# Kernel tuning notes

Hardware: AMD Instinct MI355X
Metric: run time of the kernel (lower is better)

The kernel has to match this reference:

```python
import jax, jax.numpy as jnp
import numpy as np

N_USER = 100000
N_ITEM = 50000
N = N_USER + N_ITEM
E = 1000000
D = 64
B = 4096
GAMMA = -0.45
ZETA = 1.05
LAMBDA0 = 1e-4
REG_WEIGHT = 1e-4


def setup_inputs() -> dict:
    key = jax.random.key(0)
    ks = jax.random.split(key, 20)
    s = 1.0 / np.sqrt(D)
    inp = {
        'features': jax.random.normal(ks[0], (N, D), jnp.float32) * 0.1,
        'row': jax.random.randint(ks[1], (E,), 0, N, jnp.int32),
        'col': jax.random.randint(ks[2], (E,), 0, N, jnp.int32),
        'users': jax.random.randint(ks[3], (B,), 0, N_USER, jnp.int32),
        'items': jax.random.randint(ks[4], (B,), 0, N_ITEM, jnp.int32),
        'neg_items': jax.random.randint(ks[5], (B,), 0, N_ITEM, jnp.int32),
        'u0': jax.random.uniform(ks[6], (E, 1), jnp.float32, 1e-7, 1.0 - 1e-7),
        'u1': jax.random.uniform(ks[7], (E, 1), jnp.float32, 1e-7, 1.0 - 1e-7),
        'temperature': jnp.full((1,), 0.5, jnp.float32),
        'W_nb0': jax.random.normal(ks[8], (D, D), jnp.float32) * s,
        'b_nb0': jnp.zeros((D,), jnp.float32),
        'W_self0': jax.random.normal(ks[9], (D, D), jnp.float32) * s,
        'b_self0': jnp.zeros((D,), jnp.float32),
        'W_att0': jax.random.normal(ks[10], (2 * D, 1), jnp.float32) * s,
        'b_att0': jnp.zeros((1,), jnp.float32),
        'W_nb1': jax.random.normal(ks[11], (D, D), jnp.float32) * s,
        'b_nb1': jnp.zeros((D,), jnp.float32),
        'W_self1': jax.random.normal(ks[12], (D, D), jnp.float32) * s,
        'b_self1': jnp.zeros((D,), jnp.float32),
        'W_att1': jax.random.normal(ks[13], (2 * D, 1), jnp.float32) * s,
        'b_att1': jnp.zeros((1,), jnp.float32),
    }
    return inp


def _edge_layer(x, row, col, u, Wn, bn, Ws, bs, Wa, ba, temp):
    # edge-gather attention MLP: [E, D] gathers + small GEMMs
    h_nb = jax.nn.relu(x[row] @ Wn + bn)
    h_self = jax.nn.relu(x[col] @ Ws + bs)
    log_alpha = jnp.concatenate([h_nb, h_self], axis=1) @ Wa + ba  # [E, 1]
    # hard-concrete sample (training=True): logistic noise + stretch + clip
    noise = jnp.log(u) - jnp.log1p(-u)
    gate = jax.nn.sigmoid((noise + log_alpha) / temp)
    mask = jnp.clip(gate * (ZETA - GAMMA) + GAMMA, 0.0, 1.0)[:, 0]  # [E]
    # sparse symmetric degree normalization
    rowsum = jax.ops.segment_sum(mask, row, num_segments=N) + 1e-6
    d_inv_sqrt = jnp.clip(rowsum ** -0.5, 0.0, 10.0)
    vals = mask * d_inv_sqrt[row] * d_inv_sqrt[col]
    # SpMM: x_next[r] = sum_e vals[e] * x[col[e]]
    x_next = jax.ops.segment_sum(vals[:, None] * x[col], row, num_segments=N)
    return x_next, log_alpha


def reference(features, row, col, users, items, neg_items, u0, u1, temperature,
              W_nb0, b_nb0, W_self0, b_self0, W_att0, b_att0,
              W_nb1, b_nb1, W_self1, b_self1, W_att1, b_att1):
    t = temperature[0]
    x1, w0 = _edge_layer(features, row, col, u0, W_nb0, b_nb0, W_self0, b_self0, W_att0, b_att0, t)
    x2, w1 = _edge_layer(x1, row, col, u1, W_nb1, b_nb1, W_self1, b_self1, W_att1, b_att1, t)
    xs = features + x1 + x2  # sum(embedsLst)
    x_user, x_item = xs[:N_USER], xs[N_USER:]
    anc, pos, neg = x_user[users], x_item[items], x_item[neg_items]
    pos_scores = jnp.sum(anc * pos, axis=1)
    neg_scores = jnp.sum(anc * neg, axis=1)
    bpr = -jnp.mean(jnp.log(jax.nn.sigmoid(pos_scores - neg_scores) + 1e-5))
    params = [W_nb0, b_nb0, W_self0, b_self0, W_att0, b_att0,
              W_nb1, b_nb1, W_self1, b_self1, W_att1, b_att1]
    reg = sum(jnp.sum(p * p) for p in params) * REG_WEIGHT
    lt = jnp.log(-GAMMA / ZETA)
    l0 = (jnp.mean(jax.nn.sigmoid(w0 - t * lt)) + jnp.mean(jax.nn.sigmoid(w1 - t * lt))) * LAMBDA0
    return bpr + reg + l0
```

## Files before the change

kernel.cpp:

```cpp
#include <hip/hip_runtime.h>
#include <hip/hip_bf16.h>

#define N_TOT   150000
#define N_USER  100000
#define E_TOT   1000000
#define B_TOT   4096
#define D_DIM   64

#define NSCAN_PAD   150016
#define BKT_SHIFT   10
#define BKT_ROWS    (1 << BKT_SHIFT)
#define NBKT        ((N_TOT + BKT_ROWS - 1) / BKT_ROWS)
#define BKT_CAP     8192
#define BIN_CHUNK   4096
#define NBIN_BLOCKS ((E_TOT + BIN_CHUNK - 1) / BIN_CHUNK)
#define COL_MASK    0x3FFFF

typedef short short8v  __attribute__((ext_vector_type(8)));
typedef float float4v  __attribute__((ext_vector_type(4)));

__device__ __forceinline__ float b2f(unsigned int lo16)
{
    union { unsigned int u; float f; } c; c.u = lo16 << 16; return c.f;
}
__device__ __forceinline__ unsigned short f2b(float f)
{
    union { float f; unsigned int u; } c; c.f = f;
    unsigned int u = c.u + 0x7FFFu + ((c.u >> 16) & 1u);
    return (unsigned short)(u >> 16);
}
__device__ __forceinline__ unsigned short f2h(float f)
{
    union { _Float16 h; unsigned short u; } c; c.h = (_Float16)f; return c.u;
}
__device__ __forceinline__ float h2f(unsigned short u)
{
    union { unsigned short u; _Float16 h; } c; c.u = u; return (float)c.h;
}
__device__ __forceinline__ int   f_as_i(float f) { union { float f; int i; } c; c.f = f; return c.i; }
__device__ __forceinline__ float i_as_f(int i)   { union { int i; float f; } c; c.i = i; return c.f; }

__global__ void prep_kernel(const float4* __restrict__ in, ushort4* __restrict__ out, int n4,
                            const float* __restrict__ Wn0, const float* __restrict__ Ws0,
                            const float* __restrict__ Wn1, const float* __restrict__ Ws1,
                            unsigned short* __restrict__ wpk)
{
    if (blockIdx.x < 1024) {
        for (int i = blockIdx.x * 256 + threadIdx.x; i < n4; i += 1024 * 256) {
            float4 v = in[i];
            ushort4 o;
            o.x = f2b(v.x); o.y = f2b(v.y); o.z = f2b(v.z); o.w = f2b(v.w);
            out[i] = o;
        }
        return;
    }
    int f = (blockIdx.x - 1024) * 256 + threadIdx.x;
    if (f >= 2048) return;
    const float* W[4] = {Wn0, Ws0, Wn1, Ws1};
    int m   = f >> 9;
    int rem = f & 511;
    int kb  = rem >> 8;
    int nt  = (rem >> 6) & 3;
    int l   = rem & 63;
    const float* Wm = W[m];
    int kbase = 32 * kb + ((l >> 4) << 3);
    int n     = 16 * nt + (l & 15);
    unsigned short o[8];
    #pragma unroll
    for (int j = 0; j < 8; ++j) o[j] = f2b(Wm[(kbase + j) * 64 + n]);
    ushort4* dst = (ushort4*)(wpk + (size_t)f * 8);
    dst[0] = make_ushort4(o[0], o[1], o[2], o[3]);
    dst[1] = make_ushort4(o[4], o[5], o[6], o[7]);
}

__global__ __launch_bounds__(256)
void node_scalars_mfma_kernel(const unsigned short* __restrict__ xb,
                              const unsigned short* __restrict__ wpack,
                              const float* __restrict__ bn, const float* __restrict__ bs,
                              const float* __restrict__ Wa,
                              float* __restrict__ a_nb, float* __restrict__ a_self,
                              int nNodes)
{
    const int lane = threadIdx.x & 63;
    const int wid  = (blockIdx.x * blockDim.x + threadIdx.x) >> 6;
    const int nodeBase = wid * 16;
    if (nodeBase >= nNodes) return;

    short8v bfrag[2][2][4];
    #pragma unroll
    for (int m = 0; m < 2; ++m)
        #pragma unroll
        for (int kb = 0; kb < 2; ++kb)
            #pragma unroll
            for (int nt = 0; nt < 4; ++nt)
                bfrag[m][kb][nt] =
                    *(const short8v*)(wpack + (size_t)((((m * 2 + kb) * 4 + nt) * 64 + lane)) * 8);

    const size_t rowOff = (size_t)(nodeBase + (lane & 15)) * 64 + ((lane >> 4) << 3);
    short8v a0 = *(const short8v*)(xb + rowOff);
    short8v a1 = *(const short8v*)(xb + rowOff + 32);

    float4v acc[2][4];
    #pragma unroll
    for (int m = 0; m < 2; ++m)
        #pragma unroll
        for (int nt = 0; nt < 4; ++nt) {
            float4v z = {0.f, 0.f, 0.f, 0.f};
            z = __builtin_amdgcn_mfma_f32_16x16x32_bf16(a0, bfrag[m][0][nt], z, 0, 0, 0);
            z = __builtin_amdgcn_mfma_f32_16x16x32_bf16(a1, bfrag[m][1][nt], z, 0, 0, 0);
            acc[m][nt] = z;
        }

    const int j = lane & 15;
    float pn[4] = {0.f, 0.f, 0.f, 0.f};
    float ps[4] = {0.f, 0.f, 0.f, 0.f};
    #pragma unroll
    for (int nt = 0; nt < 4; ++nt) {
        float bnv = bn[nt * 16 + j], bsv = bs[nt * 16 + j];
        float wan = Wa[nt * 16 + j], was = Wa[64 + nt * 16 + j];
        #pragma unroll
        for (int r = 0; r < 4; ++r) {
            pn[r] = fmaf(fmaxf(acc[0][nt][r] + bnv, 0.f), wan, pn[r]);
            ps[r] = fmaf(fmaxf(acc[1][nt][r] + bsv, 0.f), was, ps[r]);
        }
    }
    #pragma unroll
    for (int off = 1; off < 16; off <<= 1) {
        #pragma unroll
        for (int r = 0; r < 4; ++r) {
            pn[r] += __shfl_xor(pn[r], off);
            ps[r] += __shfl_xor(ps[r], off);
        }
    }
    if (j == 0) {
        const int g = lane >> 4;
        #pragma unroll
        for (int r = 0; r < 4; ++r) {
            int node = nodeBase + g * 4 + r;
            a_nb[node]   = pn[r];
            a_self[node] = ps[r];
        }
    }
}

__global__ __launch_bounds__(256)
void bin_kernel(const int* __restrict__ row, const int* __restrict__ col,
                const float* __restrict__ u0, const float* __restrict__ u1,
                int* __restrict__ bcnt, int2* __restrict__ tmp, int nE)
{
    __shared__ int cnt[NBKT];
    __shared__ int base[NBKT];
    for (int i = threadIdx.x; i < NBKT; i += 256) cnt[i] = 0;
    __syncthreads();

    const int e0 = blockIdx.x * BIN_CHUNK + threadIdx.x;
    int r[16], w0[16], pk[16];
    #pragma unroll
    for (int k = 0; k < 16; ++k) {
        int e = e0 + k * 256;
        r[k] = (e < nE) ? row[e] : -1;
        if (r[k] >= 0) {
            int rl = r[k] & (BKT_ROWS - 1);
            w0[k] = (rl << 18) | col[e];
            float ua = u0[e], ub = u1[e];
            float n0 = __logf(__fdividef(ua, 1.0f - ua));
            float n1 = __logf(__fdividef(ub, 1.0f - ub));
            pk[k] = (int)(((unsigned int)f2h(n1) << 16) | (unsigned int)f2h(n0));
            atomicAdd(&cnt[r[k] >> BKT_SHIFT], 1);
        }
    }
    __syncthreads();

    for (int i = threadIdx.x; i < NBKT; i += 256) {
        int cc = cnt[i];
        base[i] = cc ? atomicAdd(&bcnt[i], cc) : 0;
        cnt[i] = 0;
    }
    __syncthreads();

    #pragma unroll
    for (int k = 0; k < 16; ++k) {
        if (r[k] >= 0) {
            int b   = r[k] >> BKT_SHIFT;
            int loc = atomicAdd(&cnt[b], 1);
            tmp[(size_t)b * BKT_CAP + base[b] + loc] = make_int2(w0[k], pk[k]);
        }
    }
}

__global__ void bucket_scan_kernel(const int* __restrict__ bcnt, int* __restrict__ bbase,
                                   int* __restrict__ start)
{
    __shared__ int sh[256];
    int t = threadIdx.x;
    int v = (t < NBKT) ? bcnt[t] : 0;
    sh[t] = v;
    __syncthreads();
    for (int off = 1; off < 256; off <<= 1) {
        int x = sh[t];
        if (t >= off) x += sh[t - off];
        __syncthreads();
        sh[t] = x;
        __syncthreads();
    }
    if (t <= NBKT) bbase[t] = (t == 0) ? 0 : sh[t - 1];
    if (t == 0) start[N_TOT] = E_TOT;
}

__global__ __launch_bounds__(256)
void scatter2_kernel(const int2* __restrict__ tmp, const int* __restrict__ bcnt,
                     const int* __restrict__ bbase,
                     int* __restrict__ start, int2* __restrict__ rec)
{
    __shared__ int pref[BKT_ROWS];
    __shared__ int wsum[256];

    const int b     = blockIdx.x;
    const int rlo   = b << BKT_SHIFT;
    const int nrows = min(BKT_ROWS, N_TOT - rlo);
    const int cntb  = bcnt[b];
    const int baseb = bbase[b];
    const int t     = threadIdx.x;
    const int2* __restrict__ bkt = tmp + (size_t)b * BKT_CAP;

    for (int i = t; i < BKT_ROWS; i += 256) pref[i] = 0;
    __syncthreads();

    for (int j = t; j < cntb; j += 256)
        atomicAdd(&pref[(unsigned int)bkt[j].x >> 18], 1);
    __syncthreads();

    const int base4 = t * 4;
    int v0 = pref[base4], v1 = pref[base4 + 1], v2 = pref[base4 + 2], v3 = pref[base4 + 3];
    int s = v0 + v1 + v2 + v3;
    wsum[t] = s;
    __syncthreads();
    for (int off = 1; off < 256; off <<= 1) {
        int x = wsum[t];
        if (t >= off) x += wsum[t - off];
        __syncthreads();
        wsum[t] = x;
        __syncthreads();
    }
    const int pre = wsum[t] - s;
    const int p0 = pre, p1 = pre + v0, p2 = pre + v0 + v1, p3 = pre + v0 + v1 + v2;

    if (base4     < nrows) start[rlo + base4]     = baseb + p0;
    if (base4 + 1 < nrows) start[rlo + base4 + 1] = baseb + p1;
    if (base4 + 2 < nrows) start[rlo + base4 + 2] = baseb + p2;
    if (base4 + 3 < nrows) start[rlo + base4 + 3] = baseb + p3;

    pref[base4] = p0; pref[base4 + 1] = p1; pref[base4 + 2] = p2; pref[base4 + 3] = p3;
    __syncthreads();

    for (int j = t; j < cntb; j += 256) {
        int2 q  = bkt[j];
        int loc = atomicAdd(&pref[(unsigned int)q.x >> 18], 1);
        rec[baseb + loc] = make_int2(q.x & COL_MASK, q.y);
    }
}

__global__ __launch_bounds__(256)
void edge_pass_a_kernel(const int2* __restrict__ rec, const int* __restrict__ start,
                        const int uSel,
                        const float* __restrict__ a_nb, const float* __restrict__ a_self,
                        const float* __restrict__ ba_p, const float* __restrict__ temp_p,
                        float2* __restrict__ wc, int2* __restrict__ range,
                        float* __restrict__ dis,
                        float* __restrict__ l0_accum, int nNodes)
{
    const float ba   = ba_p[0];
    const float t    = temp_p[0];
    const float invt = 1.0f / t;
    const float lt   = logf(0.45f / 1.05f);
    const float shift = t * lt;

    const int r = blockIdx.x * 256 + threadIdx.x;
    float l0local = 0.0f;

    if (r < nNodes) {
        const int js = start[r], je = start[r + 1];
        const float la_base = a_nb[r] + ba;
        float rs = 0.0f;
        int k = js;
        for (int j = js; j < je; ++j) {
            int2 q = rec[j];
            int c = q.x;
            float la = la_base + a_self[c];
            unsigned int pk = (unsigned int)q.y;
            float noise = h2f((unsigned short)(uSel ? (pk >> 16) : (pk & 0xFFFFu)));
            float gate  = 1.0f / (1.0f + __expf(-(noise + la) * invt));
            float m = fminf(fmaxf(gate * 1.5f - 0.45f, 0.0f), 1.0f);
            rs += m;
            l0local += 1.0f / (1.0f + __expf(-(la - shift)));
            if (m > 0.0f) { wc[k] = make_float2(m, i_as_f(c)); ++k; }
        }
        range[r] = make_int2(js, k);
        dis[r] = fminf(1.0f / sqrtf(rs + 1e-6f), 10.0f);
    }

    __shared__ float red[256];
    red[threadIdx.x] = l0local;
    __syncthreads();
    for (int s = 128; s > 0; s >>= 1) {
        if (threadIdx.x < s) red[threadIdx.x] += red[threadIdx.x + s];
        __syncthreads();
    }
    if (threadIdx.x == 0) unsafeAtomicAdd(l0_accum, red[0]);
}

__global__ void edge_gather_kernel(const float2* __restrict__ wc, const int2* __restrict__ range,
                                   const float* __restrict__ dis,
                                   const unsigned short* __restrict__ xb,
                                   unsigned short* __restrict__ xnb, int nNodes)
{
    const int lane = threadIdx.x & 63;
    const int qtr  = lane >> 4;
    const int sub  = lane & 15;
    const int wave   = (blockIdx.x * blockDim.x + threadIdx.x) >> 6;
    const int nWaves = (gridDim.x * blockDim.x) >> 6;
    const int nQuads = (nNodes + 3) >> 2;

    for (int p = wave; p < nQuads; p += nWaves) {
        const int r = 4 * p + qtr;
        const bool valid = r < nNodes;
        const int rr = valid ? r : nNodes - 1;
        int2 rg  = range[rr];
        float dr = dis[rr];
        int j  = rg.x;
        int je = valid ? rg.y : rg.x;
        float a0 = 0.f, a1 = 0.f, a2 = 0.f, a3 = 0.f;
        for (; j + 4 <= je; j += 4) {
            float2 w0 = wc[j], w1 = wc[j + 1], w2 = wc[j + 2], w3 = wc[j + 3];
            int c0 = f_as_i(w0.y), c1 = f_as_i(w1.y), c2 = f_as_i(w2.y), c3 = f_as_i(w3.y);
            float s0 = w0.x * dis[c0], s1 = w1.x * dis[c1];
            float s2 = w2.x * dis[c2], s3 = w3.x * dis[c3];
            uint2 q0 = *(const uint2*)(xb + (size_t)c0 * 64 + sub * 4);
            uint2 q1 = *(const uint2*)(xb + (size_t)c1 * 64 + sub * 4);
            uint2 q2 = *(const uint2*)(xb + (size_t)c2 * 64 + sub * 4);
            uint2 q3 = *(const uint2*)(xb + (size_t)c3 * 64 + sub * 4);
            a0 = fmaf(s0, b2f(q0.x & 0xFFFFu), a0);
            a1 = fmaf(s0, b2f(q0.x >> 16),     a1);
            a2 = fmaf(s0, b2f(q0.y & 0xFFFFu), a2);
            a3 = fmaf(s0, b2f(q0.y >> 16),     a3);
            a0 = fmaf(s1, b2f(q1.x & 0xFFFFu), a0);
            a1 = fmaf(s1, b2f(q1.x >> 16),     a1);
            a2 = fmaf(s1, b2f(q1.y & 0xFFFFu), a2);
            a3 = fmaf(s1, b2f(q1.y >> 16),     a3);
            a0 = fmaf(s2, b2f(q2.x & 0xFFFFu), a0);
            a1 = fmaf(s2, b2f(q2.x >> 16),     a1);
            a2 = fmaf(s2, b2f(q2.y & 0xFFFFu), a2);
            a3 = fmaf(s2, b2f(q2.y >> 16),     a3);
            a0 = fmaf(s3, b2f(q3.x & 0xFFFFu), a0);
            a1 = fmaf(s3, b2f(q3.x >> 16),     a1);
            a2 = fmaf(s3, b2f(q3.y & 0xFFFFu), a2);
            a3 = fmaf(s3, b2f(q3.y >> 16),     a3);
        }
        for (; j < je; ++j) {
            float2 w0 = wc[j];
            int c0 = f_as_i(w0.y);
            float s0 = w0.x * dis[c0];
            uint2 q0 = *(const uint2*)(xb + (size_t)c0 * 64 + sub * 4);
            a0 = fmaf(s0, b2f(q0.x & 0xFFFFu), a0);
            a1 = fmaf(s0, b2f(q0.x >> 16),     a1);
            a2 = fmaf(s0, b2f(q0.y & 0xFFFFu), a2);
            a3 = fmaf(s0, b2f(q0.y >> 16),     a3);
        }
        if (valid) {
            uint2 o;
            o.x = ((unsigned int)f2b(a1 * dr) << 16) | (unsigned int)f2b(a0 * dr);
            o.y = ((unsigned int)f2b(a3 * dr) << 16) | (unsigned int)f2b(a2 * dr);
            *(uint2*)(xnb + (size_t)r * 64 + sub * 4) = o;
        }
    }
}

__global__ void bpr_kernel(const float* __restrict__ f,
                           const unsigned short* __restrict__ x1b,
                           const unsigned short* __restrict__ x2b,
                           const int* __restrict__ users, const int* __restrict__ items,
                           const int* __restrict__ negs,
                           float* __restrict__ bpr_accum, int B)
{
    const int lane   = threadIdx.x & 63;
    const int wave   = (blockIdx.x * blockDim.x + threadIdx.x) >> 6;
    const int nWaves = (gridDim.x * blockDim.x) >> 6;

    float local = 0.0f;
    for (int b = wave; b < B; b += nWaves) {
        size_t ui = (size_t)users[b] * 64 + lane;
        size_t pi = (size_t)(N_USER + items[b]) * 64 + lane;
        size_t ni = (size_t)(N_USER + negs[b]) * 64 + lane;
        float a = f[ui] + b2f(x1b[ui]) + b2f(x2b[ui]);
        float p = f[pi] + b2f(x1b[pi]) + b2f(x2b[pi]);
        float n = f[ni] + b2f(x1b[ni]) + b2f(x2b[ni]);
        float ps = a * p, ns = a * n;
        #pragma unroll
        for (int off = 32; off; off >>= 1) {
            ps += __shfl_xor(ps, off);
            ns += __shfl_xor(ns, off);
        }
        if (lane == 0) {
            float s = 1.0f / (1.0f + expf(-(ps - ns)));
            local += -logf(s + 1e-5f);
        }
    }
    if (lane == 0) unsafeAtomicAdd(bpr_accum, local);
}

__global__ void reg_kernel(const float* __restrict__ w0, const float* __restrict__ b0,
                           const float* __restrict__ w1, const float* __restrict__ b1,
                           const float* __restrict__ wa0, const float* __restrict__ ba0,
                           const float* __restrict__ w2, const float* __restrict__ b2,
                           const float* __restrict__ w3, const float* __restrict__ b3,
                           const float* __restrict__ wa1, const float* __restrict__ ba1,
                           float* __restrict__ accum)
{
    int t = threadIdx.x;
    float s = 0.0f;
    for (int i = t; i < 4096; i += 256)
        s += w0[i]*w0[i] + w1[i]*w1[i] + w2[i]*w2[i] + w3[i]*w3[i];
    for (int i = t; i < 64; i += 256)
        s += b0[i]*b0[i] + b1[i]*b1[i] + b2[i]*b2[i] + b3[i]*b3[i];
    for (int i = t; i < 128; i += 256)
        s += wa0[i]*wa0[i] + wa1[i]*wa1[i];
    if (t == 0) s += ba0[0]*ba0[0] + ba1[0]*ba1[0];

    __shared__ float red[256];
    red[t] = s;
    __syncthreads();
    for (int st = 128; st > 0; st >>= 1) {
        if (t < st) red[t] += red[t + st];
        __syncthreads();
    }
    if (t == 0) accum[0] = red[0];
}

__global__ void finalize_kernel(const float* __restrict__ scal, float* __restrict__ out)
{
    float bpr = scal[0] / (float)B_TOT;
    float reg = scal[1] * 1e-4f;
    float l0  = (scal[2] + scal[3]) * (1e-4f / (float)E_TOT);
    out[0] = bpr + reg + l0;
}

extern "C" void kernel_launch(void* const* d_in, const int* in_sizes, int n_in,
                              void* d_out, int out_size, void* d_ws, size_t ws_size,
                              hipStream_t stream)
{
    const float* features = (const float*)d_in[0];
    const int*   row      = (const int*)d_in[1];
    const int*   col      = (const int*)d_in[2];
    const int*   users    = (const int*)d_in[3];
    const int*   items    = (const int*)d_in[4];
    const int*   negs     = (const int*)d_in[5];
    const float* u0       = (const float*)d_in[6];
    const float* u1       = (const float*)d_in[7];
    const float* temp     = (const float*)d_in[8];
    const float* W_nb0    = (const float*)d_in[9];
    const float* b_nb0    = (const float*)d_in[10];
    const float* W_self0  = (const float*)d_in[11];
    const float* b_self0  = (const float*)d_in[12];
    const float* W_att0   = (const float*)d_in[13];
    const float* b_att0   = (const float*)d_in[14];
    const float* W_nb1    = (const float*)d_in[15];
    const float* b_nb1    = (const float*)d_in[16];
    const float* W_self1  = (const float*)d_in[17];
    const float* b_self1  = (const float*)d_in[18];
    const float* W_att1   = (const float*)d_in[19];
    const float* b_att1   = (const float*)d_in[20];
    float* out = (float*)d_out;

    float* ws = (float*)d_ws;
    unsigned short* fb  = (unsigned short*)ws;
    unsigned short* x1b = (unsigned short*)(ws + 4800000);
    unsigned short* x2b = (unsigned short*)(ws + 9600000);
    float* scal  = ws + 14400000;
    int*   bcnt  = (int*)(scal + 16);
    int*   bbase = bcnt + 160;
    int*   start = bbase + 160;
    int2*  tmp   = (int2*)(start + NSCAN_PAD);
    float2* wc   = (float2*)tmp;
    int2*  rec   = tmp + (size_t)NBKT * BKT_CAP;
    int2*  range = rec + E_TOT;
    float* dis   = (float*)(range + N_TOT);
    float* a_nb  = dis + N_TOT;
    float* a_self= a_nb + N_TOT;
    unsigned short* wpk =
        (unsigned short*)(((uintptr_t)(a_self + N_TOT) + 15) & ~(uintptr_t)15);

    hipMemsetAsync(scal, 0, (16 + 160) * sizeof(float), stream);

    const int nNodeBlocks = (N_TOT + 255) / 256;
    const int nMfmaBlocks = (N_TOT / 16 + 3) / 4;

    prep_kernel<<<1032, 256, 0, stream>>>((const float4*)features, (ushort4*)fb, N_TOT * 16,
                                          W_nb0, W_self0, W_nb1, W_self1, wpk);

    bin_kernel<<<NBIN_BLOCKS, 256, 0, stream>>>(row, col, u0, u1, bcnt, tmp, E_TOT);
    bucket_scan_kernel<<<1, 256, 0, stream>>>(bcnt, bbase, start);
    scatter2_kernel<<<NBKT, 256, 0, stream>>>(tmp, bcnt, bbase, start, rec);

    node_scalars_mfma_kernel<<<nMfmaBlocks, 256, 0, stream>>>(fb, wpk, b_nb0, b_self0, W_att0,
                                                              a_nb, a_self, N_TOT);
    edge_pass_a_kernel<<<nNodeBlocks, 256, 0, stream>>>(rec, start, 0, a_nb, a_self,
                                                        b_att0, temp, wc, range, dis,
                                                        &scal[2], N_TOT);
    edge_gather_kernel<<<2048, 256, 0, stream>>>(wc, range, dis, fb, x1b, N_TOT);

    node_scalars_mfma_kernel<<<nMfmaBlocks, 256, 0, stream>>>(x1b, wpk + 8192, b_nb1, b_self1,
                                                              W_att1, a_nb, a_self, N_TOT);
    edge_pass_a_kernel<<<nNodeBlocks, 256, 0, stream>>>(rec, start, 1, a_nb, a_self,
                                                        b_att1, temp, wc, range, dis,
                                                        &scal[3], N_TOT);
    edge_gather_kernel<<<2048, 256, 0, stream>>>(wc, range, dis, x1b, x2b, N_TOT);

    bpr_kernel<<<64, 256, 0, stream>>>(features, x1b, x2b, users, items, negs, &scal[0], B_TOT);
    reg_kernel<<<1, 256, 0, stream>>>(W_nb0, b_nb0, W_self0, b_self0, W_att0, b_att0,
                                      W_nb1, b_nb1, W_self1, b_self1, W_att1, b_att1, &scal[1]);
    finalize_kernel<<<1, 1, 0, stream>>>(scal, out);
}
```

Before: 204.3 us.

## Fold bucket scan into scatter, widen gather to 8 rows per wave, merge loss kernels

Removes the single-block bucket_scan launch by having every scatter2 block redundantly compute the bucket prefix sum in shared memory. It also merges the bpr and reg kernels into one 65-block launch. Separately, the edge gather now handles 8 nodes per wave with 8 lanes per node, each lane loading 16-byte vectors (8 bf16) instead of 8-byte ones. The intent is fewer launches and wider memory transactions, at the cost of redundant scan work per block and fewer lanes issuing each node's gathers.

```diff
diff --git a/kernel.cpp b/kernel.cpp
--- a/kernel.cpp
+++ b/kernel.cpp
@@ -188,39 +188,33 @@
     }
 }
 
-__global__ void bucket_scan_kernel(const int* __restrict__ bcnt, int* __restrict__ bbase,
-                                   int* __restrict__ start)
-{
-    __shared__ int sh[256];
-    int t = threadIdx.x;
-    int v = (t < NBKT) ? bcnt[t] : 0;
-    sh[t] = v;
-    __syncthreads();
-    for (int off = 1; off < 256; off <<= 1) {
-        int x = sh[t];
-        if (t >= off) x += sh[t - off];
-        __syncthreads();
-        sh[t] = x;
-        __syncthreads();
-    }
-    if (t <= NBKT) bbase[t] = (t == 0) ? 0 : sh[t - 1];
-    if (t == 0) start[N_TOT] = E_TOT;
-}
-
 __global__ __launch_bounds__(256)
 void scatter2_kernel(const int2* __restrict__ tmp, const int* __restrict__ bcnt,
-                     const int* __restrict__ bbase,
                      int* __restrict__ start, int2* __restrict__ rec)
 {
     __shared__ int pref[BKT_ROWS];
     __shared__ int wsum[256];
+    __shared__ int sc[256];
 
     const int b     = blockIdx.x;
     const int rlo   = b << BKT_SHIFT;
     const int nrows = min(BKT_ROWS, N_TOT - rlo);
+    const int t     = threadIdx.x;
+
+    int v = (t < NBKT) ? bcnt[t] : 0;
+    sc[t] = v;
+    __syncthreads();
+    for (int off = 1; off < 256; off <<= 1) {
+        int x = sc[t];
+        if (t >= off) x += sc[t - off];
+        __syncthreads();
+        sc[t] = x;
+        __syncthreads();
+    }
     const int cntb  = bcnt[b];
-    const int baseb = bbase[b];
-    const int t     = threadIdx.x;
+    const int baseb = (b == 0) ? 0 : sc[b - 1];
+    if (b == 0 && t == 0) start[N_TOT] = E_TOT;
+
     const int2* __restrict__ bkt = tmp + (size_t)b * BKT_CAP;
 
     for (int i = t; i < BKT_ROWS; i += 256) pref[i] = 0;
@@ -315,14 +309,14 @@
                                    unsigned short* __restrict__ xnb, int nNodes)
 {
     const int lane = threadIdx.x & 63;
-    const int qtr  = lane >> 4;
-    const int sub  = lane & 15;
+    const int oct  = lane >> 3;
+    const int sub  = lane & 7;
     const int wave   = (blockIdx.x * blockDim.x + threadIdx.x) >> 6;
     const int nWaves = (gridDim.x * blockDim.x) >> 6;
-    const int nQuads = (nNodes + 3) >> 2;
-
-    for (int p = wave; p < nQuads; p += nWaves) {
-        const int r = 4 * p + qtr;
+    const int nOcts  = (nNodes + 7) >> 3;
+
+    for (int p = wave; p < nOcts; p += nWaves) {
+        const int r = 8 * p + oct;
         const bool valid = r < nNodes;
         const int rr = valid ? r : nNodes - 1;
         int2 rg  = range[rr];
@@ -330,61 +324,92 @@
         int j  = rg.x;
         int je = valid ? rg.y : rg.x;
         float a0 = 0.f, a1 = 0.f, a2 = 0.f, a3 = 0.f;
+        float a4 = 0.f, a5 = 0.f, a6 = 0.f, a7 = 0.f;
         for (; j + 4 <= je; j += 4) {
             float2 w0 = wc[j], w1 = wc[j + 1], w2 = wc[j + 2], w3 = wc[j + 3];
             int c0 = f_as_i(w0.y), c1 = f_as_i(w1.y), c2 = f_as_i(w2.y), c3 = f_as_i(w3.y);
             float s0 = w0.x * dis[c0], s1 = w1.x * dis[c1];
             float s2 = w2.x * dis[c2], s3 = w3.x * dis[c3];
-            uint2 q0 = *(const uint2*)(xb + (size_t)c0 * 64 + sub * 4);
-            uint2 q1 = *(const uint2*)(xb + (size_t)c1 * 64 + sub * 4);
-            uint2 q2 = *(const uint2*)(xb + (size_t)c2 * 64 + sub * 4);
-            uint2 q3 = *(const uint2*)(xb + (size_t)c3 * 64 + sub * 4);
-            a0 = fmaf(s0, b2f(q0.x & 0xFFFFu), a0);
-            a1 = fmaf(s0, b2f(q0.x >> 16),     a1);
-            a2 = fmaf(s0, b2f(q0.y & 0xFFFFu), a2);
-            a3 = fmaf(s0, b2f(q0.y >> 16),     a3);
-            a0 = fmaf(s1, b2f(q1.x & 0xFFFFu), a0);
-            a1 = fmaf(s1, b2f(q1.x >> 16),     a1);
-            a2 = fmaf(s1, b2f(q1.y & 0xFFFFu), a2);
-            a3 = fmaf(s1, b2f(q1.y >> 16),     a3);
-            a0 = fmaf(s2, b2f(q2.x & 0xFFFFu), a0);
-            a1 = fmaf(s2, b2f(q2.x >> 16),     a1);
-            a2 = fmaf(s2, b2f(q2.y & 0xFFFFu), a2);
-            a3 = fmaf(s2, b2f(q2.y >> 16),     a3);
-            a0 = fmaf(s3, b2f(q3.x & 0xFFFFu), a0);
-            a1 = fmaf(s3, b2f(q3.x >> 16),     a1);
-            a2 = fmaf(s3, b2f(q3.y & 0xFFFFu), a2);
-            a3 = fmaf(s3, b2f(q3.y >> 16),     a3);
+            uint4 q0 = *(const uint4*)(xb + (size_t)c0 * 64 + sub * 8);
+            uint4 q1 = *(const uint4*)(xb + (size_t)c1 * 64 + sub * 8);
+            uint4 q2 = *(const uint4*)(xb + (size_t)c2 * 64 + sub * 8);
+            uint4 q3 = *(const uint4*)(xb + (size_t)c3 * 64 + sub * 8);
+            a0 = fmaf(s0, b2f(q0.x & 0xFFFFu), a0); a1 = fmaf(s0, b2f(q0.x >> 16), a1);
+            a2 = fmaf(s0, b2f(q0.y & 0xFFFFu), a2); a3 = fmaf(s0, b2f(q0.y >> 16), a3);
+            a4 = fmaf(s0, b2f(q0.z & 0xFFFFu), a4); a5 = fmaf(s0, b2f(q0.z >> 16), a5);
+            a6 = fmaf(s0, b2f(q0.w & 0xFFFFu), a6); a7 = fmaf(s0, b2f(q0.w >> 16), a7);
+            a0 = fmaf(s1, b2f(q1.x & 0xFFFFu), a0); a1 = fmaf(s1, b2f(q1.x >> 16), a1);
+            a2 = fmaf(s1, b2f(q1.y & 0xFFFFu), a2); a3 = fmaf(s1, b2f(q1.y >> 16), a3);
+            a4 = fmaf(s1, b2f(q1.z & 0xFFFFu), a4); a5 = fmaf(s1, b2f(q1.z >> 16), a5);
+            a6 = fmaf(s1, b2f(q1.w & 0xFFFFu), a6); a7 = fmaf(s1, b2f(q1.w >> 16), a7);
+            a0 = fmaf(s2, b2f(q2.x & 0xFFFFu), a0); a1 = fmaf(s2, b2f(q2.x >> 16), a1);
+            a2 = fmaf(s2, b2f(q2.y & 0xFFFFu), a2); a3 = fmaf(s2, b2f(q2.y >> 16), a3);
+            a4 = fmaf(s2, b2f(q2.z & 0xFFFFu), a4); a5 = fmaf(s2, b2f(q2.z >> 16), a5);
+            a6 = fmaf(s2, b2f(q2.w & 0xFFFFu), a6); a7 = fmaf(s2, b2f(q2.w >> 16), a7);
+            a0 = fmaf(s3, b2f(q3.x & 0xFFFFu), a0); a1 = fmaf(s3, b2f(q3.x >> 16), a1);
+            a2 = fmaf(s3, b2f(q3.y & 0xFFFFu), a2); a3 = fmaf(s3, b2f(q3.y >> 16), a3);
+            a4 = fmaf(s3, b2f(q3.z & 0xFFFFu), a4); a5 = fmaf(s3, b2f(q3.z >> 16), a5);
+            a6 = fmaf(s3, b2f(q3.w & 0xFFFFu), a6); a7 = fmaf(s3, b2f(q3.w >> 16), a7);
         }
         for (; j < je; ++j) {
             float2 w0 = wc[j];
             int c0 = f_as_i(w0.y);
             float s0 = w0.x * dis[c0];
-            uint2 q0 = *(const uint2*)(xb + (size_t)c0 * 64 + sub * 4);
-            a0 = fmaf(s0, b2f(q0.x & 0xFFFFu), a0);
-            a1 = fmaf(s0, b2f(q0.x >> 16),     a1);
-            a2 = fmaf(s0, b2f(q0.y & 0xFFFFu), a2);
-            a3 = fmaf(s0, b2f(q0.y >> 16),     a3);
+            uint4 q0 = *(const uint4*)(xb + (size_t)c0 * 64 + sub * 8);
+            a0 = fmaf(s0, b2f(q0.x & 0xFFFFu), a0); a1 = fmaf(s0, b2f(q0.x >> 16), a1);
+            a2 = fmaf(s0, b2f(q0.y & 0xFFFFu), a2); a3 = fmaf(s0, b2f(q0.y >> 16), a3);
+            a4 = fmaf(s0, b2f(q0.z & 0xFFFFu), a4); a5 = fmaf(s0, b2f(q0.z >> 16), a5);
+            a6 = fmaf(s0, b2f(q0.w & 0xFFFFu), a6); a7 = fmaf(s0, b2f(q0.w >> 16), a7);
         }
         if (valid) {
-            uint2 o;
+            uint4 o;
             o.x = ((unsigned int)f2b(a1 * dr) << 16) | (unsigned int)f2b(a0 * dr);
             o.y = ((unsigned int)f2b(a3 * dr) << 16) | (unsigned int)f2b(a2 * dr);
-            *(uint2*)(xnb + (size_t)r * 64 + sub * 4) = o;
-        }
-    }
-}
-
-__global__ void bpr_kernel(const float* __restrict__ f,
-                           const unsigned short* __restrict__ x1b,
-                           const unsigned short* __restrict__ x2b,
-                           const int* __restrict__ users, const int* __restrict__ items,
-                           const int* __restrict__ negs,
-                           float* __restrict__ bpr_accum, int B)
-{
-    const int lane   = threadIdx.x & 63;
-    const int wave   = (blockIdx.x * blockDim.x + threadIdx.x) >> 6;
-    const int nWaves = (gridDim.x * blockDim.x) >> 6;
+            o.z = ((unsigned int)f2b(a5 * dr) << 16) | (unsigned int)f2b(a4 * dr);
+            o.w = ((unsigned int)f2b(a7 * dr) << 16) | (unsigned int)f2b(a6 * dr);
+            *(uint4*)(xnb + (size_t)r * 64 + sub * 8) = o;
+        }
+    }
+}
+
+__global__ void loss_kernel(const float* __restrict__ f,
+                            const unsigned short* __restrict__ x1b,
+                            const unsigned short* __restrict__ x2b,
+                            const int* __restrict__ users, const int* __restrict__ items,
+                            const int* __restrict__ negs,
+                            const float* __restrict__ w0, const float* __restrict__ b0,
+                            const float* __restrict__ w1, const float* __restrict__ b1,
+                            const float* __restrict__ wa0, const float* __restrict__ ba0,
+                            const float* __restrict__ w2, const float* __restrict__ b2,
+                            const float* __restrict__ w3, const float* __restrict__ b3,
+                            const float* __restrict__ wa1, const float* __restrict__ ba1,
+                            float* __restrict__ scal, int B)
+{
+    const int t = threadIdx.x;
+    if (blockIdx.x == 64) {
+        float s = 0.0f;
+        for (int i = t; i < 4096; i += 256)
+            s += w0[i]*w0[i] + w1[i]*w1[i] + w2[i]*w2[i] + w3[i]*w3[i];
+        for (int i = t; i < 64; i += 256)
+            s += b0[i]*b0[i] + b1[i]*b1[i] + b2[i]*b2[i] + b3[i]*b3[i];
+        for (int i = t; i < 128; i += 256)
+            s += wa0[i]*wa0[i] + wa1[i]*wa1[i];
+        if (t == 0) s += ba0[0]*ba0[0] + ba1[0]*ba1[0];
+
+        __shared__ float red[256];
+        red[t] = s;
+        __syncthreads();
+        for (int st = 128; st > 0; st >>= 1) {
+            if (t < st) red[t] += red[t + st];
+            __syncthreads();
+        }
+        if (t == 0) scal[1] = red[0];
+        return;
+    }
+
+    const int lane   = t & 63;
+    const int wave   = (blockIdx.x * 256 + t) >> 6;
+    const int nWaves = (64 * 256) >> 6;
 
     float local = 0.0f;
     for (int b = wave; b < B; b += nWaves) {
@@ -405,35 +430,7 @@
             local += -logf(s + 1e-5f);
         }
     }
-    if (lane == 0) unsafeAtomicAdd(bpr_accum, local);
-}
-
-__global__ void reg_kernel(const float* __restrict__ w0, const float* __restrict__ b0,
-                           const float* __restrict__ w1, const float* __restrict__ b1,
-                           const float* __restrict__ wa0, const float* __restrict__ ba0,
-                           const float* __restrict__ w2, const float* __restrict__ b2,
-                           const float* __restrict__ w3, const float* __restrict__ b3,
-                           const float* __restrict__ wa1, const float* __restrict__ ba1,
-                           float* __restrict__ accum)
-{
-    int t = threadIdx.x;
-    float s = 0.0f;
-    for (int i = t; i < 4096; i += 256)
-        s += w0[i]*w0[i] + w1[i]*w1[i] + w2[i]*w2[i] + w3[i]*w3[i];
-    for (int i = t; i < 64; i += 256)
-        s += b0[i]*b0[i] + b1[i]*b1[i] + b2[i]*b2[i] + b3[i]*b3[i];
-    for (int i = t; i < 128; i += 256)
-        s += wa0[i]*wa0[i] + wa1[i]*wa1[i];
-    if (t == 0) s += ba0[0]*ba0[0] + ba1[0]*ba1[0];
-
-    __shared__ float red[256];
-    red[t] = s;
-    __syncthreads();
-    for (int st = 128; st > 0; st >>= 1) {
-        if (t < st) red[t] += red[t + st];
-        __syncthreads();
-    }
-    if (t == 0) accum[0] = red[0];
+    if (lane == 0) unsafeAtomicAdd(&scal[0], local);
 }
 
 __global__ void finalize_kernel(const float* __restrict__ scal, float* __restrict__ out)
@@ -477,8 +474,7 @@
     unsigned short* x2b = (unsigned short*)(ws + 9600000);
     float* scal  = ws + 14400000;
     int*   bcnt  = (int*)(scal + 16);
-    int*   bbase = bcnt + 160;
-    int*   start = bbase + 160;
+    int*   start = bcnt + 160;
     int2*  tmp   = (int2*)(start + NSCAN_PAD);
     float2* wc   = (float2*)tmp;
     int2*  rec   = tmp + (size_t)NBKT * BKT_CAP;
@@ -498,8 +494,7 @@
                                           W_nb0, W_self0, W_nb1, W_self1, wpk);
 
     bin_kernel<<<NBIN_BLOCKS, 256, 0, stream>>>(row, col, u0, u1, bcnt, tmp, E_TOT);
-    bucket_scan_kernel<<<1, 256, 0, stream>>>(bcnt, bbase, start);
-    scatter2_kernel<<<NBKT, 256, 0, stream>>>(tmp, bcnt, bbase, start, rec);
+    scatter2_kernel<<<NBKT, 256, 0, stream>>>(tmp, bcnt, start, rec);
 
     node_scalars_mfma_kernel<<<nMfmaBlocks, 256, 0, stream>>>(fb, wpk, b_nb0, b_self0, W_att0,
                                                               a_nb, a_self, N_TOT);
@@ -515,8 +510,9 @@
                                                         &scal[3], N_TOT);
     edge_gather_kernel<<<2048, 256, 0, stream>>>(wc, range, dis, x1b, x2b, N_TOT);
 
-    bpr_kernel<<<64, 256, 0, stream>>>(features, x1b, x2b, users, items, negs, &scal[0], B_TOT);
-    reg_kernel<<<1, 256, 0, stream>>>(W_nb0, b_nb0, W_self0, b_self0, W_att0, b_att0,
-                                      W_nb1, b_nb1, W_self1, b_self1, W_att1, b_att1, &scal[1]);
+    loss_kernel<<<65, 256, 0, stream>>>(features, x1b, x2b, users, items, negs,
+                                        W_nb0, b_nb0, W_self0, b_self0, W_att0, b_att0,
+                                        W_nb1, b_nb1, W_self1, b_self1, W_att1, b_att1,
+                                        scal, B_TOT);
     finalize_kernel<<<1, 1, 0, stream>>>(scal, out);
 }
```

New measurement: 184.7 us. 9.6% less time.
